# Optimization experiments

Hardware: AMD Instinct MI355X
Metric: run time of the kernel (lower is better)

Reference implementation:

```python
import jax, jax.numpy as jnp
import numpy as np

N = 131072      # active sites
NIN = 32        # input channels
FV = 27         # filter volume (3^3)
NOUT = NIN * FV # 864


def setup_inputs() -> dict:
    key = jax.random.key(0)
    k1, k2 = jax.random.split(key)
    features = jax.random.normal(k1, (N, NIN), dtype=jnp.float32)
    # rules[k, i] = input row index for output site i at filter offset k;
    # value N is a sentinel meaning 'no active neighbor' -> contributes zeros.
    rules = jax.random.randint(k2, (FV, N), 0, N + 1, dtype=jnp.int64)
    # ShapeContext registers weight = eye(nOut).view(filter_volume, nIn, nOut)
    weight = jnp.eye(NOUT, dtype=jnp.float32).reshape(FV, NIN, NOUT)
    bias = jnp.zeros((NOUT,), dtype=jnp.float32)
    return {"features": features, "weight": weight, "bias": bias, "rules": rules}


def reference(features, weight, bias, rules):
    # Pad with a zero row so sentinel index N gathers zeros (missing neighbor).
    padded = jnp.concatenate([features, jnp.zeros((1, features.shape[1]), features.dtype)], axis=0)
    gathered = padded[rules]                     # [FV, N, NIN] gather via rulebook
    # Per-offset matmul and accumulate (scatter is identity here since each
    # output site has exactly one slot per offset).
    out = jnp.einsum('kni,kio->no', gathered, weight) + bias  # [N, NOUT]
    return out
```

## Files before the change

kernel.cpp:

```cpp
#include <hip/hip_runtime.h>


#define N_SITES 131072
#define NIN 32
#define FV 27
#define NOUT 864
#define F4_PER_SITE 216
#define TOTAL_F4 (N_SITES * (long long)F4_PER_SITE)
#define ELEMS 4

typedef float f32x4 __attribute__((ext_vector_type(4)));

__global__ __launch_bounds__(256) void shape_context_gather(
    const float* __restrict__ features,
    const float* __restrict__ bias,
    const int*   __restrict__ rules,
    float*       __restrict__ out)
{
    const unsigned base = blockIdx.x * (256u * ELEMS) + threadIdx.x;

    int      r[ELEMS];
    unsigned jj[ELEMS];
    f32x4    v[ELEMS];

    #pragma unroll
    for (int i = 0; i < ELEMS; ++i) {
        unsigned tid = base + i * 256u;
        unsigned n = tid / F4_PER_SITE;
        unsigned j = tid - n * F4_PER_SITE;
        unsigned k = j >> 3;
        jj[i] = j;
        r[i] = rules[k * (unsigned)N_SITES + n];
    }

    #pragma unroll
    for (int i = 0; i < ELEMS; ++i) {
        bool valid = (unsigned)r[i] < (unsigned)N_SITES;
        unsigned rr = valid ? (unsigned)r[i] : 0u;
        v[i] = ((const f32x4*)features)[rr * 8u + (jj[i] & 7u)];
        if (!valid) v[i] = (f32x4){0.f, 0.f, 0.f, 0.f};
    }

    #pragma unroll
    for (int i = 0; i < ELEMS; ++i) {
        f32x4 o = v[i] + ((const f32x4*)bias)[jj[i]];
        __builtin_nontemporal_store(o, ((f32x4*)out) + (base + i * 256u));
    }
}

extern "C" void kernel_launch(void* const* d_in, const int* in_sizes, int n_in,
                              void* d_out, int out_size, void* d_ws, size_t ws_size,
                              hipStream_t stream) {
    const float* features = (const float*)d_in[0];
    const float* bias     = (const float*)d_in[2];
    const int*   rules    = (const int*)d_in[3];
    float*       out      = (float*)d_out;

    const long long total   = TOTAL_F4;
    const int       threads = 256;
    const int       blocks  = (int)(total / (threads * ELEMS));

    shape_context_gather<<<blocks, threads, 0, stream>>>(features, bias, rules, out);
}
```

Baseline: 511.6 us.

## Bucket-sort rulebook pairs by input row before gathering features

Replaces the single direct gather kernel with a multi-kernel pipeline: a histogram of rule targets into 256 row buckets, a scan, and a scatter into a workspace-sorted pair list. A final gather kernel walks the pairs bucket by bucket, so feature reads are localized. The cost is extra passes over the rules, several kernel launches, and output writes that become scattered 128-byte chunks instead of fully sequential stores. It falls back to the original kernel when the workspace is too small.

```diff
diff --git a/kernel.cpp b/kernel.cpp
--- a/kernel.cpp
+++ b/kernel.cpp
@@ -5,44 +5,143 @@
 #define NIN 32
 #define FV 27
 #define NOUT 864
-#define F4_PER_SITE 216
-#define TOTAL_F4 (N_SITES * (long long)F4_PER_SITE)
-#define ELEMS 4
+#define PAIRS (FV * N_SITES)
+#define NBUCKET 256
+#define BUCKET_SHIFT 9
+#define EPB 256
+#define NBLK4 ((PAIRS + NBUCKET * (EPB - 1)) / EPB)
+#define SORT_CAP (NBLK4 * EPB)
+#define HBLOCKS (PAIRS / 4096)
+#define SKIP_PIDX 0x3FFFFFu
+
+#define WS_SORTED 0ull
+#define WS_BHIST  14416896ull
+#define WS_BBASE  15301632ull
+#define WS_BBUCK  15302912ull
+#define WS_NEEDED (15302912ull + 4ull * NBLK4)
 
 typedef float f32x4 __attribute__((ext_vector_type(4)));
 
+__global__ __launch_bounds__(256) void k0_prefill(unsigned* __restrict__ sorted) {
+    unsigned i = blockIdx.x * 256u + threadIdx.x;
+    sorted[i] = SKIP_PIDX;
+}
+
+__global__ __launch_bounds__(256) void k1_hist(const int* __restrict__ rules,
+                                               unsigned* __restrict__ blockHist) {
+    __shared__ unsigned hist[NBUCKET];
+    hist[threadIdx.x] = 0u;
+    __syncthreads();
+    unsigned base0 = blockIdx.x * 4096u;
+    #pragma unroll
+    for (int j = 0; j < 16; ++j) {
+        int r = rules[base0 + j * 256u + threadIdx.x];
+        unsigned b = ((unsigned)r < (unsigned)N_SITES) ? ((unsigned)r >> BUCKET_SHIFT) : 0u;
+        atomicAdd(&hist[b], 1u);
+    }
+    __syncthreads();
+    blockHist[blockIdx.x * NBUCKET + threadIdx.x] = hist[threadIdx.x];
+}
+
+__global__ __launch_bounds__(256) void k2_scan(unsigned* __restrict__ blockHist,
+                                               unsigned* __restrict__ bucketBase,
+                                               unsigned* __restrict__ blockBucket) {
+    __shared__ unsigned tot[NBUCKET];
+    __shared__ unsigned base[NBUCKET + 1];
+    int b = threadIdx.x;
+    unsigned s = 0;
+    for (int g = 0; g < HBLOCKS; ++g) s += blockHist[g * NBUCKET + b];
+    tot[b] = s;
+    __syncthreads();
+    if (b == 0) {
+        unsigned acc = 0;
+        for (int i = 0; i < NBUCKET; ++i) {
+            base[i] = acc;
+            acc += (tot[i] + (EPB - 1)) & ~(unsigned)(EPB - 1);
+        }
+        base[NBUCKET] = acc;
+    }
+    __syncthreads();
+    unsigned off = base[b];
+    for (int g = 0; g < HBLOCKS; ++g) {
+        unsigned t = blockHist[g * NBUCKET + b];
+        blockHist[g * NBUCKET + b] = off;
+        off += t;
+    }
+    bucketBase[b] = base[b];
+    if (b == 0) bucketBase[NBUCKET] = base[NBUCKET];
+    for (unsigned p = base[b] / EPB; p < base[b + 1] / EPB; ++p) blockBucket[p] = (unsigned)b;
+}
+
+__global__ __launch_bounds__(256) void k3_scatter(const int* __restrict__ rules,
+                                                  const unsigned* __restrict__ blockStart,
+                                                  unsigned* __restrict__ sorted) {
+    __shared__ unsigned cur[NBUCKET];
+    cur[threadIdx.x] = blockStart[blockIdx.x * NBUCKET + threadIdx.x];
+    __syncthreads();
+    unsigned base0 = blockIdx.x * 4096u;
+    #pragma unroll
+    for (int j = 0; j < 16; ++j) {
+        unsigned idx = base0 + j * 256u + threadIdx.x;
+        int r = rules[idx];
+        bool valid = (unsigned)r < (unsigned)N_SITES;
+        unsigned b = valid ? ((unsigned)r >> BUCKET_SHIFT) : 0u;
+        unsigned pos = atomicAdd(&cur[b], 1u);
+        sorted[pos] = ((unsigned)valid << 31) | (((unsigned)r & 511u) << 22) | idx;
+    }
+}
+
+__global__ __launch_bounds__(256) void k4_gather(const unsigned* __restrict__ sorted,
+                                                 const unsigned* __restrict__ blockBucket,
+                                                 const float* __restrict__ features,
+                                                 const float* __restrict__ bias,
+                                                 float* __restrict__ out) {
+    unsigned bucket = blockBucket[blockIdx.x];
+    unsigned e = threadIdx.x >> 3;
+    unsigned c = threadIdx.x & 7;
+    unsigned base0 = blockIdx.x * (unsigned)EPB;
+    #pragma unroll
+    for (int i = 0; i < EPB / 32; ++i) {
+        unsigned entry = __builtin_nontemporal_load(sorted + base0 + i * 32u + e);
+        unsigned pidx = entry & SKIP_PIDX;
+        if (pidx < (unsigned)PAIRS) {
+            unsigned valid = entry >> 31;
+            unsigned r = (bucket << BUCKET_SHIFT) | ((entry >> 22) & 511u);
+            r = valid ? r : 0u;
+            f32x4 v = ((const f32x4*)features)[(size_t)r * 8u + c];
+            if (!valid) v = (f32x4){0.f, 0.f, 0.f, 0.f};
+            unsigned n = pidx & (N_SITES - 1);
+            unsigned k = pidx >> 17;
+            v += ((const f32x4*)bias)[k * 8u + c];
+            __builtin_nontemporal_store(v, ((f32x4*)out) + ((size_t)n * 216u + k * 8u + c));
+        }
+    }
+}
+
+#define F4_PER_SITE 216
+#define TOTAL_F4 (N_SITES * (long long)F4_PER_SITE)
 __global__ __launch_bounds__(256) void shape_context_gather(
-    const float* __restrict__ features,
-    const float* __restrict__ bias,
-    const int*   __restrict__ rules,
-    float*       __restrict__ out)
-{
-    const unsigned base = blockIdx.x * (256u * ELEMS) + threadIdx.x;
-
-    int      r[ELEMS];
-    unsigned jj[ELEMS];
-    f32x4    v[ELEMS];
-
+    const float* __restrict__ features, const float* __restrict__ bias,
+    const int* __restrict__ rules, float* __restrict__ out) {
+    const unsigned base = blockIdx.x * 1024u + threadIdx.x;
+    int r[4]; unsigned jj[4]; f32x4 v[4];
     #pragma unroll
-    for (int i = 0; i < ELEMS; ++i) {
+    for (int i = 0; i < 4; ++i) {
         unsigned tid = base + i * 256u;
         unsigned n = tid / F4_PER_SITE;
         unsigned j = tid - n * F4_PER_SITE;
-        unsigned k = j >> 3;
         jj[i] = j;
-        r[i] = rules[k * (unsigned)N_SITES + n];
+        r[i] = rules[(j >> 3) * (unsigned)N_SITES + n];
     }
-
     #pragma unroll
-    for (int i = 0; i < ELEMS; ++i) {
+    for (int i = 0; i < 4; ++i) {
         bool valid = (unsigned)r[i] < (unsigned)N_SITES;
         unsigned rr = valid ? (unsigned)r[i] : 0u;
         v[i] = ((const f32x4*)features)[rr * 8u + (jj[i] & 7u)];
         if (!valid) v[i] = (f32x4){0.f, 0.f, 0.f, 0.f};
     }
-
     #pragma unroll
-    for (int i = 0; i < ELEMS; ++i) {
+    for (int i = 0; i < 4; ++i) {
         f32x4 o = v[i] + ((const f32x4*)bias)[jj[i]];
         __builtin_nontemporal_store(o, ((f32x4*)out) + (base + i * 256u));
     }
@@ -56,9 +155,20 @@
     const int*   rules    = (const int*)d_in[3];
     float*       out      = (float*)d_out;
 
-    const long long total   = TOTAL_F4;
-    const int       threads = 256;
-    const int       blocks  = (int)(total / (threads * ELEMS));
+    if (ws_size < (size_t)WS_NEEDED || d_ws == nullptr) {
+        shape_context_gather<<<(int)(TOTAL_F4 / 1024), 256, 0, stream>>>(features, bias, rules, out);
+        return;
+    }
 
-    shape_context_gather<<<blocks, threads, 0, stream>>>(features, bias, rules, out);
+    char* ws = (char*)d_ws;
+    unsigned* sorted      = (unsigned*)(ws + WS_SORTED);
+    unsigned* blockHist   = (unsigned*)(ws + WS_BHIST);
+    unsigned* bucketBase  = (unsigned*)(ws + WS_BBASE);
+    unsigned* blockBucket = (unsigned*)(ws + WS_BBUCK);
+
+    k0_prefill<<<NBLK4, 256, 0, stream>>>(sorted);
+    k1_hist<<<HBLOCKS, 256, 0, stream>>>(rules, blockHist);
+    k2_scan<<<1, 256, 0, stream>>>(blockHist, bucketBase, blockBucket);
+    k3_scatter<<<HBLOCKS, 256, 0, stream>>>(rules, blockHist, sorted);
+    k4_gather<<<NBLK4, 256, 0, stream>>>(sorted, blockBucket, features, bias, out);
 }
```

New measurement: 593.0 us. 15.9% more time.
